# Performance work log

Hardware: AMD Instinct MI355X
Metric: run time of the kernel (lower is better)

The kernel has to match this reference:

```python
import jax, jax.numpy as jnp
import numpy as np

B, N_CLOUD, QUERY_DIM = 16384, 256, 2048
NUM_PROMPT, PROMPT_DIM, HIDDEN, OUT_DIM = 1024, 1024, 64, 64
NUM_SELECT = 32
EPS = 1e-12


def setup_inputs() -> dict:
    key = jax.random.key(0)
    ks = jax.random.split(key, 8)
    return {
        "cloud": jax.random.normal(ks[0], (B, N_CLOUD, 3), dtype=jnp.float32),
        "query": jax.random.normal(ks[1], (B, QUERY_DIM), dtype=jnp.float32),
        "keys": jax.random.normal(ks[2], (NUM_PROMPT, QUERY_DIM), dtype=jnp.float32),
        "prompts": jax.random.normal(ks[3], (NUM_PROMPT, PROMPT_DIM), dtype=jnp.float32),
        "w1": jax.random.normal(ks[4], (HIDDEN, PROMPT_DIM), dtype=jnp.float32) * (1.0 / np.sqrt(PROMPT_DIM)),
        "b1": jnp.zeros((HIDDEN,), dtype=jnp.float32),
        "w2": jax.random.normal(ks[5], (OUT_DIM, HIDDEN), dtype=jnp.float32) * (1.0 / np.sqrt(HIDDEN)),
        "b2": jnp.zeros((OUT_DIM,), dtype=jnp.float32),
        "num_select": NUM_SELECT,
    }


def _l2norm(x):
    # F.normalize(x, dim=-1): x / max(||x||, eps)
    n = jnp.sqrt(jnp.sum(x * x, axis=-1, keepdims=True))
    return x / jnp.maximum(n, EPS)


def reference(cloud, query, keys, prompts, w1, b1, w2, b2, num_select):
    # cosine distance in [0,1]: (1 - cos) / 2  -> [B, num_prompt]
    dist = (1.0 - jnp.einsum("bq,nq->bn", _l2norm(query), _l2norm(keys))) * 0.5
    # eval mode: frequency == ones, so topk directly on dist (k smallest, ascending)
    neg_vals, sel_idx = jax.lax.top_k(-dist, num_select)      # [B, k]
    selected_dist = -neg_vals                                  # ascending smallest dists
    score = jax.nn.softmax(1.0 - selected_dist, axis=-1)       # [B, k]
    selected_prompts = prompts[sel_idx]                        # [B, k, prompt_dim]
    # torch.mean of score-weighted prompts over the select dim
    avg_prompt = jnp.mean(score[..., None] * selected_prompts, axis=1)  # [B, prompt_dim]
    h = jax.nn.relu(avg_prompt @ w1.T + b1)                    # [B, 64]
    o = h @ w2.T + b2                                          # [B, out_dim]
    n_pts = cloud.shape[1]
    x = jnp.broadcast_to(o[:, None, :], (o.shape[0], n_pts, o.shape[1]))  # repeat over cloud points
    return x, selected_dist
```

## Files before the change

### kernel.cpp

```cpp
#include <hip/hip_runtime.h>
#include <stdint.h>

#define B_ROWS 16384
#define NCLOUD 256
#define QDIM   2048
#define NPROMPT 1024
#define HID    64
#define ODIM   64
#define NSEL   32

typedef unsigned short u16;
typedef unsigned long long u64;
typedef __attribute__((ext_vector_type(8))) short short8;
typedef __attribute__((ext_vector_type(4))) float f32x4;

__device__ __forceinline__ u16 f2bf(float x) {
  unsigned u = __float_as_uint(x);
  unsigned r = (u + 0x7fffu + ((u >> 16) & 1u)) >> 16;
  return (u16)r;
}
__device__ __forceinline__ float bf2f(u16 h) {
  return __uint_as_float(((unsigned)h) << 16);
}

__global__ __launch_bounds__(256) void norm_split_kernel(
    const float* __restrict__ in, u16* __restrict__ out) {
  const int row = blockIdx.x;
  const int t = threadIdx.x;
  const float* rp = in + (size_t)row * QDIM;
  float4 v0 = ((const float4*)rp)[t];
  float4 v1 = ((const float4*)rp)[t + 256];
  float ss = v0.x*v0.x + v0.y*v0.y + v0.z*v0.z + v0.w*v0.w
           + v1.x*v1.x + v1.y*v1.y + v1.z*v1.z + v1.w*v1.w;
  #pragma unroll
  for (int m = 1; m < 64; m <<= 1) ss += __shfl_xor(ss, m, 64);
  __shared__ float red[4];
  if ((t & 63) == 0) red[t >> 6] = ss;
  __syncthreads();
  float tot = red[0] + red[1] + red[2] + red[3];
  float inv = 1.0f / fmaxf(sqrtf(tot), 1e-12f);
  float x0[4] = {v0.x, v0.y, v0.z, v0.w};
  float x1[4] = {v1.x, v1.y, v1.z, v1.w};
  u16 h0[4], h1[4], l0[4], l1[4];
  #pragma unroll
  for (int j = 0; j < 4; ++j) {
    float a = x0[j] * inv;
    h0[j] = f2bf(a); l0[j] = f2bf(a - bf2f(h0[j]));
    float b = x1[j] * inv;
    h1[j] = f2bf(b); l1[j] = f2bf(b - bf2f(h1[j]));
  }
  u16* ob = out + (size_t)row * (2 * QDIM);
  *(ushort4*)(ob + t * 4)               = *(const ushort4*)h0;
  *(ushort4*)(ob + 1024 + t * 4)        = *(const ushort4*)h1;
  *(ushort4*)(ob + QDIM + t * 4)        = *(const ushort4*)l0;
  *(ushort4*)(ob + QDIM + 1024 + t * 4) = *(const ushort4*)l1;
}

__global__ __launch_bounds__(256) void p1_kernel(
    const float* __restrict__ prompts, const float* __restrict__ w1,
    float* __restrict__ P1) {
  const int n = blockIdx.x;
  const int wid = threadIdx.x >> 6, lane = threadIdx.x & 63;
  const float4* pr = (const float4*)(prompts + (size_t)n * 1024);
  for (int hb = 0; hb < 16; ++hb) {
    const int h = hb * 4 + wid;
    const float4* wr = (const float4*)(w1 + (size_t)h * 1024);
    float acc = 0.f;
    #pragma unroll
    for (int i = 0; i < 4; ++i) {
      float4 a = pr[i * 64 + lane];
      float4 b = wr[i * 64 + lane];
      acc += a.x * b.x + a.y * b.y + a.z * b.z + a.w * b.w;
    }
    #pragma unroll
    for (int s = 1; s < 64; s <<= 1) acc += __shfl_xor(acc, s, 64);
    if (lane == 0) P1[(size_t)n * 64 + h] = acc;
  }
}

__global__ __launch_bounds__(256) void gemm_split_kernel(
    const u16* __restrict__ A, const u16* __restrict__ B,
    float* __restrict__ S) {
  __shared__ u16 sA[128][64];
  __shared__ u16 sB[128][64];

  const int flat = blockIdx.y * 8 + blockIdx.x;
  const int v = (flat & 7) * 128 + (flat >> 3);
  const int bx = v & 7, by = v >> 3;
  const int m0 = by * 128, n0 = bx * 128;

  const int tid = threadIdx.x;
  const int lane = tid & 63, w = tid >> 6;
  const int wrow = w >> 1, wcol = w & 1;

  f32x4 acc[4][4] = {};

  const int srow = w * 32 + (lane >> 3);
  const int scol = (lane & 7) * 8;

  for (int kt = 0; kt < 96; ++kt) {
    const int term = kt >> 5;
    const int ko = (kt & 31) * 64;
    const int acol = ((term == 2) ? 2048 : 0) + ko;
    const int bcol = ((term == 1) ? 2048 : 0) + ko;
    #pragma unroll
    for (int c = 0; c < 4; ++c) {
      const int r = srow + c * 8;
      const u16* gp = A + (size_t)(m0 + r) * 4096 + acol + scol;
      __builtin_amdgcn_global_load_lds(
          (const __attribute__((address_space(1))) void*)gp,
          (__attribute__((address_space(3))) void*)&sA[r][scol], 16, 0, 0);
    }
    #pragma unroll
    for (int c = 0; c < 4; ++c) {
      const int r = srow + c * 8;
      const u16* gp = B + (size_t)(n0 + r) * 4096 + bcol + scol;
      __builtin_amdgcn_global_load_lds(
          (const __attribute__((address_space(1))) void*)gp,
          (__attribute__((address_space(3))) void*)&sB[r][scol], 16, 0, 0);
    }
    __syncthreads();
    #pragma unroll
    for (int ks = 0; ks < 2; ++ks) {
      const int kk = ks * 32 + (lane >> 4) * 8;
      short8 aF[4], bF[4];
      #pragma unroll
      for (int mi = 0; mi < 4; ++mi)
        aF[mi] = *(const short8*)&sA[wrow * 64 + mi * 16 + (lane & 15)][kk];
      #pragma unroll
      for (int ni = 0; ni < 4; ++ni)
        bF[ni] = *(const short8*)&sB[wcol * 64 + ni * 16 + (lane & 15)][kk];
      #pragma unroll
      for (int mi = 0; mi < 4; ++mi)
        #pragma unroll
        for (int ni = 0; ni < 4; ++ni)
          acc[mi][ni] = __builtin_amdgcn_mfma_f32_16x16x32_bf16(
              aF[mi], bF[ni], acc[mi][ni], 0, 0, 0);
    }
    __syncthreads();
  }
  const int crow0 = m0 + wrow * 64 + (lane >> 4) * 4;
  const int ccol0 = n0 + wcol * 64 + (lane & 15);
  #pragma unroll
  for (int mi = 0; mi < 4; ++mi)
    #pragma unroll
    for (int ni = 0; ni < 4; ++ni)
      #pragma unroll
      for (int r = 0; r < 4; ++r)
        S[(size_t)(crow0 + mi * 16 + r) * 1024 + ccol0 + ni * 16] =
            0.5f - 0.5f * acc[mi][ni][r];
}

__global__ __launch_bounds__(256) void topk_mlp_bcast_kernel(
    const float* __restrict__ S, const float* __restrict__ P1,
    const float* __restrict__ b1, const float* __restrict__ w2,
    const float* __restrict__ b2, float* __restrict__ xout,
    float* __restrict__ sdout) {
  const int wid = threadIdx.x >> 6;
  const int lane = threadIdx.x & 63;
  const int b = blockIdx.x * 4 + wid;

  const float* Sr = S + (size_t)b * NPROMPT;
  u64 k[16];
  #pragma unroll
  for (int i = 0; i < 4; ++i) {
    float4 v = ((const float4*)Sr)[i * 64 + lane];
    const int base = (i * 64 + lane) * 4;
    float vv[4] = {v.x, v.y, v.z, v.w};
    #pragma unroll
    for (int j = 0; j < 4; ++j) {
      unsigned u = __float_as_uint(vv[j]);
      u = (u & 0x80000000u) ? ~u : (u | 0x80000000u);
      k[i * 4 + j] = ((u64)u << 32) | (unsigned)(base + j);
    }
  }
  u64 m = k[0];
  #pragma unroll
  for (int i = 1; i < 16; ++i) m = (k[i] < m) ? k[i] : m;

  u64 sel = 0;
  for (int r = 0; r < NSEL; ++r) {
    u64 g = m;
    #pragma unroll
    for (int s = 1; s < 64; s <<= 1) {
      u64 o = __shfl_xor(g, s, 64);
      g = (o < g) ? o : g;
    }
    if ((lane & 31) == r) sel = g;
    if (m == g) {
      #pragma unroll
      for (int i = 0; i < 16; ++i)
        if (k[i] == g) k[i] = 0xFFFFFFFFFFFFFFFFull;
      m = k[0];
      #pragma unroll
      for (int i = 1; i < 16; ++i) m = (k[i] < m) ? k[i] : m;
    }
  }

  unsigned u = (unsigned)(sel >> 32);
  unsigned bits = (u & 0x80000000u) ? (u ^ 0x80000000u) : ~u;
  float d = __uint_as_float(bits);
  int idx = (int)(sel & 0xffffffffu);
  if (lane < NSEL) sdout[(size_t)b * NSEL + lane] = d;

  float d0 = __shfl(d, 0, 32);
  float e = __expf(d0 - d);
  float sum = e;
  #pragma unroll
  for (int s = 1; s < 32; s <<= 1) sum += __shfl_xor(sum, s, 32);
  float score = e / sum;

  float acc = 0.f;
  #pragma unroll
  for (int r = 0; r < NSEL; ++r) {
    float sr = __shfl(score, r, 32);
    int ir = __shfl(idx, r, 32);
    acc = fmaf(sr, P1[(size_t)ir * HID + lane], acc);
  }
  float h = fmaxf(acc * (1.0f / NSEL) + b1[lane], 0.0f);

  float o = b2[lane];
  #pragma unroll
  for (int hh = 0; hh < 64; ++hh)
    o = fmaf(__shfl(h, hh, 64), w2[lane * HID + hh], o);

  const int src = (lane & 15) * 4;
  float4 f;
  f.x = __shfl(o, src + 0, 64);
  f.y = __shfl(o, src + 1, 64);
  f.z = __shfl(o, src + 2, 64);
  f.w = __shfl(o, src + 3, 64);
  float4* xr = (float4*)(xout + (size_t)b * (NCLOUD * ODIM));
  #pragma unroll 4
  for (int i = 0; i < 64; ++i) xr[i * 64 + lane] = f;
}

extern "C" void kernel_launch(void* const* d_in, const int* in_sizes, int n_in,
                              void* d_out, int out_size, void* d_ws, size_t ws_size,
                              hipStream_t stream) {
  const float* query   = (const float*)d_in[1];
  const float* keys    = (const float*)d_in[2];
  const float* prompts = (const float*)d_in[3];
  const float* w1      = (const float*)d_in[4];
  const float* b1      = (const float*)d_in[5];
  const float* w2      = (const float*)d_in[6];
  const float* b2      = (const float*)d_in[7];

  char* ws = (char*)d_ws;
  u16*   Abig = (u16*)ws;
  u16*   Bbig = (u16*)(ws + 134217728);
  float* P1   = (float*)(ws + 134217728 + 8388608);
  float* S    = (float*)(ws + 134217728 + 8388608 + 262144);

  float* xout  = (float*)d_out;
  float* sdout = (float*)d_out + (size_t)B_ROWS * NCLOUD * ODIM;

  norm_split_kernel<<<B_ROWS, 256, 0, stream>>>(query, Abig);
  norm_split_kernel<<<NPROMPT, 256, 0, stream>>>(keys, Bbig);
  p1_kernel<<<NPROMPT, 256, 0, stream>>>(prompts, w1, P1);
  gemm_split_kernel<<<dim3(8, 128), 256, 0, stream>>>(Abig, Bbig, S);
  topk_mlp_bcast_kernel<<<B_ROWS / 4, 256, 0, stream>>>(S, P1, b1, w2, b2, xout, sdout);
}
```

Before: 1.567 ms.

## Rewrite split-bf16 GEMM as pipelined 256x256 tile kernel and simplify top-k keys

The GEMM moves from 128x128 tiles with 256 threads and a sync per k-step to 256x256 tiles with 512 threads. It uses eight half-tile LDS slots with XOR-swizzled layout, and global-to-LDS loads for later k-steps are issued while MFMAs run on the current ones, using explicit waitcnt, barriers and setprio. This targets global load latency, LDS bank conflicts and operand reuse. Separately, the top-k kernel switches from 64-bit packed value/index keys to 32-bit value keys with a second shuffle-min reduction for the index, to cut 64-bit shuffle cost. The GEMM grid shrinks to 256 blocks, which may underfill the GPU, and the hand-tuned wait counts are fragile.

```diff
diff --git a/kernel.cpp b/kernel.cpp
--- a/kernel.cpp
+++ b/kernel.cpp
@@ -10,6 +10,7 @@
 #define NSEL   32
 
 typedef unsigned short u16;
+typedef unsigned int u32;
 typedef unsigned long long u64;
 typedef __attribute__((ext_vector_type(8))) short short8;
 typedef __attribute__((ext_vector_type(4))) float f32x4;
@@ -78,71 +79,126 @@
   }
 }
 
-__global__ __launch_bounds__(256) void gemm_split_kernel(
+#define FENCE() asm volatile("" ::: "memory")
+#define BARRIER() do { FENCE(); __builtin_amdgcn_s_barrier(); FENCE(); } while (0)
+
+__device__ __forceinline__ void stage_half(const u16* __restrict__ gbase,
+                                           int grow0, int gcol0,
+                                           u16* slot, int tid) {
+  #pragma unroll
+  for (int sel = 0; sel < 2; ++sel) {
+    const int o = sel * 8192 + tid * 16;
+    const int row = o >> 7;
+    const int c = o & 127;
+    const int cs = c ^ ((row & 7) << 4);
+    const u16* src = gbase + (size_t)(grow0 + row) * 4096 + gcol0 + (cs >> 1);
+    __builtin_amdgcn_global_load_lds(
+        (const __attribute__((address_space(1))) void*)src,
+        (__attribute__((address_space(3))) void*)((char*)slot + o), 16, 0, 0);
+  }
+}
+
+__device__ __forceinline__ int kcolA(int kt) {
+  return ((kt >> 5) == 2 ? 2048 : 0) + (kt & 31) * 64;
+}
+__device__ __forceinline__ int kcolB(int kt) {
+  return ((kt >> 5) == 1 ? 2048 : 0) + (kt & 31) * 64;
+}
+
+__global__ __launch_bounds__(512, 2) void gemm8p_kernel(
     const u16* __restrict__ A, const u16* __restrict__ B,
     float* __restrict__ S) {
-  __shared__ u16 sA[128][64];
-  __shared__ u16 sB[128][64];
-
-  const int flat = blockIdx.y * 8 + blockIdx.x;
-  const int v = (flat & 7) * 128 + (flat >> 3);
-  const int bx = v & 7, by = v >> 3;
-  const int m0 = by * 128, n0 = bx * 128;
+  __shared__ u16 sH[8][8192];
+
+  const int flat = blockIdx.x;
+  const int v = (flat & 7) * 32 + (flat >> 3);
+  const int bn = v & 3, bm = v >> 2;
+  const int m0 = bm * 256, n0 = bn * 256;
 
   const int tid = threadIdx.x;
   const int lane = tid & 63, w = tid >> 6;
-  const int wrow = w >> 1, wcol = w & 1;
-
-  f32x4 acc[4][4] = {};
-
-  const int srow = w * 32 + (lane >> 3);
-  const int scol = (lane & 7) * 8;
-
-  for (int kt = 0; kt < 96; ++kt) {
-    const int term = kt >> 5;
-    const int ko = (kt & 31) * 64;
-    const int acol = ((term == 2) ? 2048 : 0) + ko;
-    const int bcol = ((term == 1) ? 2048 : 0) + ko;
-    #pragma unroll
-    for (int c = 0; c < 4; ++c) {
-      const int r = srow + c * 8;
-      const u16* gp = A + (size_t)(m0 + r) * 4096 + acol + scol;
-      __builtin_amdgcn_global_load_lds(
-          (const __attribute__((address_space(1))) void*)gp,
-          (__attribute__((address_space(3))) void*)&sA[r][scol], 16, 0, 0);
-    }
-    #pragma unroll
-    for (int c = 0; c < 4; ++c) {
-      const int r = srow + c * 8;
-      const u16* gp = B + (size_t)(n0 + r) * 4096 + bcol + scol;
-      __builtin_amdgcn_global_load_lds(
-          (const __attribute__((address_space(1))) void*)gp,
-          (__attribute__((address_space(3))) void*)&sB[r][scol], 16, 0, 0);
-    }
-    __syncthreads();
-    #pragma unroll
-    for (int ks = 0; ks < 2; ++ks) {
-      const int kk = ks * 32 + (lane >> 4) * 8;
-      short8 aF[4], bF[4];
+  const int wm = w >> 2, wn = w & 3;
+  const int l15 = lane & 15, l16 = lane >> 4;
+  const int axor = (l15 & 7) << 4;
+  const int acol0 = ((0 * 64 + l16 * 16) ^ axor) >> 1;
+  const int acol1 = ((1 * 64 + l16 * 16) ^ axor) >> 1;
+  const int arow = l15 * 64;
+  const int bbase = ((wn & 1) * 64 + l15) * 64;
+
+  f32x4 acc[8][4] = {};
+
+  stage_half(A, m0 + 0 * 128, kcolA(0), sH[0], tid);
+  stage_half(A, m0 + 1 * 128, kcolA(0), sH[1], tid);
+  stage_half(B, n0 + 0 * 128, kcolB(0), sH[4], tid);
+  stage_half(B, n0 + 1 * 128, kcolB(0), sH[5], tid);
+  stage_half(B, n0 + 0 * 128, kcolB(1), sH[6], tid);
+  stage_half(B, n0 + 1 * 128, kcolB(1), sH[7], tid);
+  asm volatile("s_waitcnt vmcnt(4)" ::: "memory");
+  BARRIER();
+
+  for (int i = 0; i < 48; ++i) {
+    const int t1 = 2 * i + 1;
+    const int kA1 = kcolA(t1);
+    const int kB2 = kcolB(min(2 * i + 2, 95));
+    const int kA2 = kcolA(min(2 * i + 2, 95));
+    const int kB3 = kcolB(min(2 * i + 3, 95));
+
+    #pragma unroll
+    for (int blk = 0; blk < 2; ++blk) {
+      const u16* aslot = sH[blk * 2 + wm];
+      const u16* bslot = sH[4 + blk * 2 + (wn >> 1)];
+      short8 bF[4][2];
       #pragma unroll
-      for (int mi = 0; mi < 4; ++mi)
-        aF[mi] = *(const short8*)&sA[wrow * 64 + mi * 16 + (lane & 15)][kk];
-      #pragma unroll
-      for (int ni = 0; ni < 4; ++ni)
-        bF[ni] = *(const short8*)&sB[wcol * 64 + ni * 16 + (lane & 15)][kk];
-      #pragma unroll
-      for (int mi = 0; mi < 4; ++mi)
+      for (int q = 0; q < 4; ++q) {
+        if (q == 0) {
+          #pragma unroll
+          for (int ni = 0; ni < 4; ++ni) {
+            bF[ni][0] = *(const short8*)(bslot + bbase + ni * 1024 + acol0);
+            bF[ni][1] = *(const short8*)(bslot + bbase + ni * 1024 + acol1);
+          }
+        }
+        short8 aF[2][2];
+        #pragma unroll
+        for (int dm = 0; dm < 2; ++dm) {
+          aF[dm][0] = *(const short8*)(aslot + (2 * q + dm) * 1024 + arow + acol0);
+          aF[dm][1] = *(const short8*)(aslot + (2 * q + dm) * 1024 + arow + acol1);
+        }
+        if (blk == 0) {
+          if (q == 0) stage_half(A, m0 + 0 * 128, kA1, sH[2], tid);
+          if (q == 1) stage_half(A, m0 + 1 * 128, kA1, sH[3], tid);
+          if (q == 2) stage_half(B, n0 + 0 * 128, kB2, sH[4], tid);
+          if (q == 3) stage_half(B, n0 + 1 * 128, kB2, sH[5], tid);
+        } else {
+          if (q == 0) stage_half(A, m0 + 0 * 128, kA2, sH[0], tid);
+          if (q == 1) stage_half(A, m0 + 1 * 128, kA2, sH[1], tid);
+          if (q == 2) stage_half(B, n0 + 0 * 128, kB3, sH[6], tid);
+          if (q == 3) stage_half(B, n0 + 1 * 128, kB3, sH[7], tid);
+        }
+        if (q == 3) asm volatile("s_waitcnt vmcnt(4)" ::: "memory");
+        BARRIER();
+        asm volatile("s_waitcnt lgkmcnt(0)" ::: "memory");
+        __builtin_amdgcn_sched_barrier(0);
+        __builtin_amdgcn_s_setprio(1);
         #pragma unroll
         for (int ni = 0; ni < 4; ++ni)
-          acc[mi][ni] = __builtin_amdgcn_mfma_f32_16x16x32_bf16(
-              aF[mi], bF[ni], acc[mi][ni], 0, 0, 0);
-    }
-    __syncthreads();
-  }
-  const int crow0 = m0 + wrow * 64 + (lane >> 4) * 4;
-  const int ccol0 = n0 + wcol * 64 + (lane & 15);
-  #pragma unroll
-  for (int mi = 0; mi < 4; ++mi)
+          #pragma unroll
+          for (int s = 0; s < 2; ++s) {
+            acc[2 * q][ni] = __builtin_amdgcn_mfma_f32_16x16x32_bf16(
+                aF[0][s], bF[ni][s], acc[2 * q][ni], 0, 0, 0);
+            acc[2 * q + 1][ni] = __builtin_amdgcn_mfma_f32_16x16x32_bf16(
+                aF[1][s], bF[ni][s], acc[2 * q + 1][ni], 0, 0, 0);
+          }
+        __builtin_amdgcn_s_setprio(0);
+        BARRIER();
+      }
+    }
+  }
+  asm volatile("s_waitcnt vmcnt(0)" ::: "memory");
+
+  const int crow0 = m0 + wm * 128 + l16 * 4;
+  const int ccol0 = n0 + wn * 64 + l15;
+  #pragma unroll
+  for (int mi = 0; mi < 8; ++mi)
     #pragma unroll
     for (int ni = 0; ni < 4; ++ni)
       #pragma unroll
@@ -161,50 +217,51 @@
   const int b = blockIdx.x * 4 + wid;
 
   const float* Sr = S + (size_t)b * NPROMPT;
-  u64 k[16];
+  u32 vkey[16];
   #pragma unroll
   for (int i = 0; i < 4; ++i) {
-    float4 v = ((const float4*)Sr)[i * 64 + lane];
-    const int base = (i * 64 + lane) * 4;
-    float vv[4] = {v.x, v.y, v.z, v.w};
+    float4 vv = ((const float4*)Sr)[i * 64 + lane];
+    float f[4] = {vv.x, vv.y, vv.z, vv.w};
     #pragma unroll
     for (int j = 0; j < 4; ++j) {
-      unsigned u = __float_as_uint(vv[j]);
-      u = (u & 0x80000000u) ? ~u : (u | 0x80000000u);
-      k[i * 4 + j] = ((u64)u << 32) | (unsigned)(base + j);
-    }
-  }
-  u64 m = k[0];
-  #pragma unroll
-  for (int i = 1; i < 16; ++i) m = (k[i] < m) ? k[i] : m;
-
-  u64 sel = 0;
+      u32 u = __float_as_uint(f[j]);
+      vkey[i * 4 + j] = (u & 0x80000000u) ? ~u : (u | 0x80000000u);
+    }
+  }
+  const u32 ib = (u32)lane * 4u;
+
+  float seld = 0.f;
+  int selidx = 0;
   for (int r = 0; r < NSEL; ++r) {
-    u64 g = m;
-    #pragma unroll
-    for (int s = 1; s < 64; s <<= 1) {
-      u64 o = __shfl_xor(g, s, 64);
-      g = (o < g) ? o : g;
-    }
-    if ((lane & 31) == r) sel = g;
-    if (m == g) {
-      #pragma unroll
-      for (int i = 0; i < 16; ++i)
-        if (k[i] == g) k[i] = 0xFFFFFFFFFFFFFFFFull;
-      m = k[0];
-      #pragma unroll
-      for (int i = 1; i < 16; ++i) m = (k[i] < m) ? k[i] : m;
-    }
-  }
-
-  unsigned u = (unsigned)(sel >> 32);
-  unsigned bits = (u & 0x80000000u) ? (u ^ 0x80000000u) : ~u;
-  float d = __uint_as_float(bits);
-  int idx = (int)(sel & 0xffffffffu);
-  if (lane < NSEL) sdout[(size_t)b * NSEL + lane] = d;
-
-  float d0 = __shfl(d, 0, 32);
-  float e = __expf(d0 - d);
+    u32 lm = vkey[0];
+    #pragma unroll
+    for (int s = 1; s < 16; ++s) lm = min(lm, vkey[s]);
+    u32 g = lm;
+    #pragma unroll
+    for (int m = 1; m < 64; m <<= 1) g = min(g, (u32)__shfl_xor((int)g, m, 64));
+    u32 li = 0xFFFFFFFFu;
+    #pragma unroll
+    for (int s = 15; s >= 0; --s)
+      li = (vkey[s] == g) ? ((u32)(s >> 2) * 256u + ib + (u32)(s & 3)) : li;
+    u32 gi = li;
+    #pragma unroll
+    for (int m = 1; m < 64; m <<= 1) gi = min(gi, (u32)__shfl_xor((int)gi, m, 64));
+    if ((lane & 31) == r) {
+      u32 bits = (g & 0x80000000u) ? (g ^ 0x80000000u) : ~g;
+      seld = __uint_as_float(bits);
+      selidx = (int)gi;
+    }
+    #pragma unroll
+    for (int s = 0; s < 16; ++s) {
+      u32 myidx = (u32)(s >> 2) * 256u + ib + (u32)(s & 3);
+      if (vkey[s] == g && myidx == gi) vkey[s] = 0xFFFFFFFFu;
+    }
+  }
+
+  if (lane < NSEL) sdout[(size_t)b * NSEL + lane] = seld;
+
+  float d0 = __shfl(seld, 0, 32);
+  float e = __expf(d0 - seld);
   float sum = e;
   #pragma unroll
   for (int s = 1; s < 32; s <<= 1) sum += __shfl_xor(sum, s, 32);
@@ -214,7 +271,7 @@
   #pragma unroll
   for (int r = 0; r < NSEL; ++r) {
     float sr = __shfl(score, r, 32);
-    int ir = __shfl(idx, r, 32);
+    int ir = __shfl(selidx, r, 32);
     acc = fmaf(sr, P1[(size_t)ir * HID + lane], acc);
   }
   float h = fmaxf(acc * (1.0f / NSEL) + b1[lane], 0.0f);
@@ -258,6 +315,6 @@
   norm_split_kernel<<<B_ROWS, 256, 0, stream>>>(query, Abig);
   norm_split_kernel<<<NPROMPT, 256, 0, stream>>>(keys, Bbig);
   p1_kernel<<<NPROMPT, 256, 0, stream>>>(prompts, w1, P1);
-  gemm_split_kernel<<<dim3(8, 128), 256, 0, stream>>>(Abig, Bbig, S);
+  gemm8p_kernel<<<256, 512, 0, stream>>>(Abig, Bbig, S);
   topk_mlp_bcast_kernel<<<B_ROWS / 4, 256, 0, stream>>>(S, P1, b1, w2, b2, xout, sdout);
 }
```

After: 1.411 ms. -9.9%, faster.
